# Kernel optimization log

Measured on AMD Instinct MI355X. Metric: run time of the kernel, lower is better.

## Reference

```python
import jax, jax.numpy as jnp
import numpy as np

EPS = 1e-13

def dct_basis(n):
    # Orthonormal DCT-II basis: C[k, i] = s_k * cos(pi*(2i+1)*k / (2n))
    k = np.arange(n)[:, None]
    i = np.arange(n)[None, :]
    C = np.cos(np.pi * (2 * i + 1) * k / (2 * n))
    scale = np.full((n, 1), np.sqrt(2.0 / n))
    scale[0, 0] = np.sqrt(1.0 / n)
    return jnp.asarray(C * scale, dtype=jnp.float32)


def setup_inputs() -> dict:
    key = jax.random.key(0)
    B, C, H, W = 128, 3, 256, 256
    inputs = jax.random.normal(key, (B, C, H, W), dtype=jnp.float32)
    mean = jnp.asarray(-8.0, dtype=jnp.float32)
    std = jnp.asarray(6.0, dtype=jnp.float32)
    return {"inputs": inputs, "mean": mean, "std": std}


def reference(inputs, mean, std):
    H, W = inputs.shape[-2], inputs.shape[-1]
    CH = dct_basis(H)  # [H, H]
    CW = dct_basis(W)  # [W, W]
    # 2D DCT-II (ortho): out[..., k1, k2] = sum_ij CH[k1,i] * x[..., i, j] * CW[k2,j]
    x = jnp.einsum('hi,bcij,wj->bchw', CH, inputs, CW)
    x = jnp.log(jnp.abs(x) + EPS)
    return (x - mean) / std
```

## Files before the change

### kernel.cpp

```cpp
#include <hip/hip_runtime.h>
#include <cmath>


#define HN    256
#define NIMG  384

__global__ void basis_init(float* __restrict__ Tdf) {
    int idx = blockIdx.x * 256 + threadIdx.x;
    int i = idx >> 8, k = idx & 255;
    double c = cos(M_PI * (2.0 * i + 1.0) * (double)k / 512.0);
    double s = (k == 0) ? sqrt(1.0 / 256.0) : sqrt(2.0 / 256.0);
    Tdf[idx] = (float)(c * s);
}

__global__ __launch_bounds__(256, 4) void t1_kernel(
    const float* __restrict__ X, const float* __restrict__ Tdf,
    float* __restrict__ T1)
{
    __shared__ float Xs[8][64];
    __shared__ float CHs[8][HN];

    const int t   = threadIdx.x;
    const int img = blockIdx.x >> 2;
    const int js  = (blockIdx.x & 3) * 64;
    const float* __restrict__ Xi = X + (size_t)img * (HN * HN);

    const int ci = t & 15;
    const int ib = t >> 4;

    float acc[4][4][4];
    #pragma unroll
    for (int s = 0; s < 4; ++s)
        #pragma unroll
        for (int r = 0; r < 4; ++r)
            #pragma unroll
            for (int jr = 0; jr < 4; ++jr) acc[s][r][jr] = 0.0f;

    for (int i0 = 0; i0 < HN; i0 += 8) {
        {
            int rr = t >> 5, cc = (t & 31) * 2;
            float2 v = *(const float2*)(Xi + (i0 + rr) * HN + js + cc);
            Xs[rr][cc] = v.x; Xs[rr][cc + 1] = v.y;
            #pragma unroll
            for (int rep = 0; rep < 2; ++rep) {
                int idx = rep * 1024 + t * 4;
                int row = idx >> 8, col = idx & 255;
                *(float4*)&CHs[row][col] =
                    *(const float4*)(Tdf + (i0 + row) * HN + col);
            }
        }
        __syncthreads();
        #pragma unroll
        for (int ii = 0; ii < 8; ++ii) {
            float xv[4];
            *(float4*)xv = *(const float4*)&Xs[ii][4 * ci];
            float ch[4][4];
            #pragma unroll
            for (int s = 0; s < 4; ++s)
                *(float4*)ch[s] = *(const float4*)&CHs[ii][64 * s + 4 * ib];
            #pragma unroll
            for (int s = 0; s < 4; ++s)
                #pragma unroll
                for (int r = 0; r < 4; ++r)
                    #pragma unroll
                    for (int jr = 0; jr < 4; ++jr)
                        acc[s][r][jr] = fmaf(ch[s][r], xv[jr], acc[s][r][jr]);
        }
        __syncthreads();
    }

    float* __restrict__ T1i = T1 + (size_t)img * (HN * HN);
    #pragma unroll
    for (int s = 0; s < 4; ++s)
        #pragma unroll
        for (int r = 0; r < 4; ++r)
            *(float4*)(T1i + (64 * s + 4 * ib + r) * HN + js + 4 * ci) =
                *(const float4*)acc[s][r];
}

__global__ __launch_bounds__(256, 4) void y_kernel(
    const float* __restrict__ T1, const float* __restrict__ Tdf,
    const float* __restrict__ meanp, const float* __restrict__ stdp,
    float* __restrict__ out)
{
    __shared__ float T1c[64][9];
    __shared__ float Bc[8][HN];

    const int t   = threadIdx.x;
    const int img = blockIdx.x >> 2;
    const int ks  = (blockIdx.x & 3) * 64;
    const float* __restrict__ T1i = T1 + (size_t)img * (HN * HN);

    const int ci = t & 15;
    const int ib = t >> 4;

    float acc[4][4][4];
    #pragma unroll
    for (int s = 0; s < 4; ++s)
        #pragma unroll
        for (int r = 0; r < 4; ++r)
            #pragma unroll
            for (int c = 0; c < 4; ++c) acc[s][r][c] = 0.0f;

    for (int j0 = 0; j0 < HN; j0 += 8) {
        {
            int rr = t >> 2, cc = (t & 3) * 2;
            float2 v = *(const float2*)(T1i + (ks + rr) * HN + j0 + cc);
            T1c[rr][cc] = v.x; T1c[rr][cc + 1] = v.y;
            #pragma unroll
            for (int rep = 0; rep < 2; ++rep) {
                int idx = rep * 1024 + t * 4;
                int row = idx >> 8, col = idx & 255;
                *(float4*)&Bc[row][col] =
                    *(const float4*)(Tdf + (j0 + row) * HN + col);
            }
        }
        __syncthreads();
        #pragma unroll
        for (int p = 0; p < 8; ++p) {
            float a[4];
            #pragma unroll
            for (int r = 0; r < 4; ++r) a[r] = T1c[4 * ib + r][p];
            float b[4][4];
            #pragma unroll
            for (int s = 0; s < 4; ++s)
                *(float4*)b[s] = *(const float4*)&Bc[p][64 * s + 4 * ci];
            #pragma unroll
            for (int s = 0; s < 4; ++s)
                #pragma unroll
                for (int r = 0; r < 4; ++r)
                    #pragma unroll
                    for (int c = 0; c < 4; ++c)
                        acc[s][r][c] = fmaf(a[r], b[s][c], acc[s][r][c]);
        }
        __syncthreads();
    }

    const float mean = meanp[0];
    const float stdv = stdp[0];
    float* __restrict__ O = out + (size_t)img * (HN * HN);
    #pragma unroll
    for (int s = 0; s < 4; ++s)
        #pragma unroll
        for (int r = 0; r < 4; ++r) {
            float4 v;
            v.x = (logf(fabsf(acc[s][r][0]) + 1e-13f) - mean) / stdv;
            v.y = (logf(fabsf(acc[s][r][1]) + 1e-13f) - mean) / stdv;
            v.z = (logf(fabsf(acc[s][r][2]) + 1e-13f) - mean) / stdv;
            v.w = (logf(fabsf(acc[s][r][3]) + 1e-13f) - mean) / stdv;
            *(float4*)(O + (ks + 4 * ib + r) * HN + 64 * s + 4 * ci) = v;
        }
}

#define SLAB 32
__global__ __launch_bounds__(256, 3) void dct2_f32(
    const float* __restrict__ X, const float* __restrict__ Tdf,
    const float* __restrict__ meanp, const float* __restrict__ stdp,
    float* __restrict__ out)
{
    __shared__ union SU {
        struct { float Xs[8][HN]; float CHc[8][SLAB]; } p1;
        float Bc[16][HN];
    } u;
    __shared__ float T1s[SLAB][HN + 1];

    const int t   = threadIdx.x;
    const int img = blockIdx.x >> 3;
    const int k0  = (blockIdx.x & 7) * SLAB;
    const float* __restrict__ Xi = X + (size_t)img * (HN * HN);
    const int ci = t & 7;
    const int ib = t >> 3;

    float acc[8][4];
    #pragma unroll
    for (int q = 0; q < 8; ++q)
        #pragma unroll
        for (int r = 0; r < 4; ++r) acc[q][r] = 0.0f;

    for (int i0 = 0; i0 < HN; i0 += 8) {
        {
            int rr = t >> 5, cc = (t & 31) * 4;
            float4 a = *(const float4*)(Xi + (i0 + rr) * HN + cc);
            float4 b = *(const float4*)(Xi + (i0 + rr) * HN + cc + 128);
            *(float4*)&u.p1.Xs[rr][cc]       = a;
            *(float4*)&u.p1.Xs[rr][cc + 128] = b;
            u.p1.CHc[rr][t & 31] = Tdf[(i0 + rr) * HN + k0 + (t & 31)];
        }
        __syncthreads();
        #pragma unroll
        for (int ii = 0; ii < 8; ++ii) {
            float xr[8];
            *(float4*)&xr[0] = *(const float4*)&u.p1.Xs[ii][8 * ib];
            *(float4*)&xr[4] = *(const float4*)&u.p1.Xs[ii][8 * ib + 4];
            float ch[4];
            *(float4*)&ch[0] = *(const float4*)&u.p1.CHc[ii][4 * ci];
            #pragma unroll
            for (int q = 0; q < 8; ++q)
                #pragma unroll
                for (int r = 0; r < 4; ++r)
                    acc[q][r] = fmaf(ch[r], xr[q], acc[q][r]);
        }
        __syncthreads();
    }
    #pragma unroll
    for (int q = 0; q < 8; ++q)
        #pragma unroll
        for (int r = 0; r < 4; ++r)
            T1s[4 * ci + r][8 * ib + q] = acc[q][r];
    __syncthreads();

    float acc2[8][4];
    #pragma unroll
    for (int q = 0; q < 8; ++q)
        #pragma unroll
        for (int r = 0; r < 4; ++r) acc2[q][r] = 0.0f;

    for (int j0 = 0; j0 < HN; j0 += 16) {
        #pragma unroll
        for (int rep = 0; rep < 4; ++rep) {
            int idx = rep * 1024 + t * 4;
            int p = idx >> 8, c = idx & 255;
            *(float4*)&u.Bc[p][c] = *(const float4*)(Tdf + (j0 + p) * HN + c);
        }
        __syncthreads();
        #pragma unroll
        for (int p = 0; p < 16; ++p) {
            float a[4];
            #pragma unroll
            for (int r = 0; r < 4; ++r) a[r] = T1s[4 * ci + r][j0 + p];
            float b[8];
            *(float4*)&b[0] = *(const float4*)&u.Bc[p][8 * ib];
            *(float4*)&b[4] = *(const float4*)&u.Bc[p][8 * ib + 4];
            #pragma unroll
            for (int q = 0; q < 8; ++q)
                #pragma unroll
                for (int r = 0; r < 4; ++r)
                    acc2[q][r] = fmaf(a[r], b[q], acc2[q][r]);
        }
        __syncthreads();
    }

    const float mean = meanp[0];
    const float stdv = stdp[0];
    #pragma unroll
    for (int q = 0; q < 8; ++q)
        #pragma unroll
        for (int r = 0; r < 4; ++r) {
            float v = (logf(fabsf(acc2[q][r]) + 1e-13f) - mean) / stdv;
            T1s[4 * ci + r][8 * ib + q] = v;
        }
    __syncthreads();

    float* __restrict__ O = out + (size_t)img * (HN * HN) + (size_t)k0 * HN;
    #pragma unroll
    for (int rep = 0; rep < 8; ++rep) {
        int idx = rep * 1024 + t * 4;
        int row = idx >> 8, col = idx & 255;
        float4 v = make_float4(T1s[row][col], T1s[row][col + 1],
                               T1s[row][col + 2], T1s[row][col + 3]);
        *(float4*)(O + row * HN + col) = v;
    }
}

extern "C" void kernel_launch(void* const* d_in, const int* in_sizes, int n_in,
                              void* d_out, int out_size, void* d_ws, size_t ws_size,
                              hipStream_t stream) {
    const float* X     = (const float*)d_in[0];
    const float* meanp = (const float*)d_in[1];
    const float* stdp  = (const float*)d_in[2];

    float* Tdf = (float*)d_ws;
    const size_t T1_OFF    = 256 * 1024;
    const size_t T1_BYTES  = (size_t)NIMG * HN * HN * sizeof(float);

    basis_init<<<256, 256, 0, stream>>>(Tdf);

    if (ws_size >= T1_OFF + T1_BYTES) {
        float* T1 = (float*)((char*)d_ws + T1_OFF);
        t1_kernel<<<NIMG * 4, 256, 0, stream>>>(X, Tdf, T1);
        y_kernel <<<NIMG * 4, 256, 0, stream>>>(T1, Tdf, meanp, stdp,
                                                (float*)d_out);
    } else {
        dct2_f32<<<NIMG * 8, 256, 0, stream>>>(X, Tdf, meanp, stdp,
                                               (float*)d_out);
    }
}
```

Measured before the change: 448.9 us.

## Register-prefetch next K-tile, double K-step to 16, transpose T1 tile in LDS

Both GEMM kernels now load the next K-slab from global memory into registers while the current slab in shared memory is being computed, with wider float4 global loads. The K step per iteration goes from 8 to 16, halving the number of barrier pairs. In y_kernel the T1 tile is stored transposed with padding so each thread reads its four A values with a single float4 LDS load. The cost is more registers for the prefetch buffers and a larger shared-memory footprint, which may reduce occupancy under the launch bounds of 4 blocks.

```diff
diff --git a/kernel.cpp b/kernel.cpp
--- a/kernel.cpp
+++ b/kernel.cpp
@@ -17,8 +17,8 @@
     const float* __restrict__ X, const float* __restrict__ Tdf,
     float* __restrict__ T1)
 {
-    __shared__ float Xs[8][64];
-    __shared__ float CHs[8][HN];
+    __shared__ float Xs[16][64];
+    __shared__ float CHs[16][HN];
 
     const int t   = threadIdx.x;
     const int img = blockIdx.x >> 2;
@@ -36,22 +36,33 @@
             #pragma unroll
             for (int jr = 0; jr < 4; ++jr) acc[s][r][jr] = 0.0f;
 
-    for (int i0 = 0; i0 < HN; i0 += 8) {
-        {
-            int rr = t >> 5, cc = (t & 31) * 2;
-            float2 v = *(const float2*)(Xi + (i0 + rr) * HN + js + cc);
-            Xs[rr][cc] = v.x; Xs[rr][cc + 1] = v.y;
-            #pragma unroll
-            for (int rep = 0; rep < 2; ++rep) {
-                int idx = rep * 1024 + t * 4;
-                int row = idx >> 8, col = idx & 255;
-                *(float4*)&CHs[row][col] =
-                    *(const float4*)(Tdf + (i0 + row) * HN + col);
-            }
-        }
-        __syncthreads();
-        #pragma unroll
-        for (int ii = 0; ii < 8; ++ii) {
+    float4 pX, pC[4];
+    const int xr_row = t >> 4, xr_col = (t & 15) * 4;
+    #define T1_PREFETCH(i0)                                                  \
+        do {                                                                 \
+            pX = *(const float4*)(Xi + ((i0) + xr_row) * HN + js + xr_col);  \
+            _Pragma("unroll")                                                \
+            for (int rep = 0; rep < 4; ++rep) {                              \
+                int idx = rep * 1024 + t * 4;                                \
+                pC[rep] = *(const float4*)(Tdf + ((i0) + (idx >> 8)) * HN    \
+                                           + (idx & 255));                   \
+            }                                                                \
+        } while (0)
+
+    T1_PREFETCH(0);
+    for (int i0 = 0; i0 < HN; i0 += 16) {
+        __syncthreads();
+        *(float4*)&Xs[xr_row][xr_col] = pX;
+        #pragma unroll
+        for (int rep = 0; rep < 4; ++rep) {
+            int idx = rep * 1024 + t * 4;
+            *(float4*)&CHs[idx >> 8][idx & 255] = pC[rep];
+        }
+        __syncthreads();
+        if (i0 + 16 < HN) T1_PREFETCH(i0 + 16);
+
+        #pragma unroll
+        for (int ii = 0; ii < 16; ++ii) {
             float xv[4];
             *(float4*)xv = *(const float4*)&Xs[ii][4 * ci];
             float ch[4][4];
@@ -66,8 +77,8 @@
                     for (int jr = 0; jr < 4; ++jr)
                         acc[s][r][jr] = fmaf(ch[s][r], xv[jr], acc[s][r][jr]);
         }
-        __syncthreads();
-    }
+    }
+    #undef T1_PREFETCH
 
     float* __restrict__ T1i = T1 + (size_t)img * (HN * HN);
     #pragma unroll
@@ -83,8 +94,8 @@
     const float* __restrict__ meanp, const float* __restrict__ stdp,
     float* __restrict__ out)
 {
-    __shared__ float T1c[64][9];
-    __shared__ float Bc[8][HN];
+    __shared__ float Ts[16][68];
+    __shared__ float Bc[16][HN];
 
     const int t   = threadIdx.x;
     const int img = blockIdx.x >> 2;
@@ -102,25 +113,38 @@
             #pragma unroll
             for (int c = 0; c < 4; ++c) acc[s][r][c] = 0.0f;
 
-    for (int j0 = 0; j0 < HN; j0 += 8) {
-        {
-            int rr = t >> 2, cc = (t & 3) * 2;
-            float2 v = *(const float2*)(T1i + (ks + rr) * HN + j0 + cc);
-            T1c[rr][cc] = v.x; T1c[rr][cc + 1] = v.y;
-            #pragma unroll
-            for (int rep = 0; rep < 2; ++rep) {
-                int idx = rep * 1024 + t * 4;
-                int row = idx >> 8, col = idx & 255;
-                *(float4*)&Bc[row][col] =
-                    *(const float4*)(Tdf + (j0 + row) * HN + col);
-            }
-        }
-        __syncthreads();
-        #pragma unroll
-        for (int p = 0; p < 8; ++p) {
+    float4 pT, pB[4];
+    const int tr_row = t >> 2, tr_col = (t & 3) * 4;
+    #define Y_PREFETCH(j0)                                                   \
+        do {                                                                 \
+            pT = *(const float4*)(T1i + (ks + tr_row) * HN + (j0) + tr_col); \
+            _Pragma("unroll")                                                \
+            for (int rep = 0; rep < 4; ++rep) {                              \
+                int idx = rep * 1024 + t * 4;                                \
+                pB[rep] = *(const float4*)(Tdf + ((j0) + (idx >> 8)) * HN    \
+                                           + (idx & 255));                   \
+            }                                                                \
+        } while (0)
+
+    Y_PREFETCH(0);
+    for (int j0 = 0; j0 < HN; j0 += 16) {
+        __syncthreads();
+        Ts[tr_col + 0][tr_row] = pT.x;
+        Ts[tr_col + 1][tr_row] = pT.y;
+        Ts[tr_col + 2][tr_row] = pT.z;
+        Ts[tr_col + 3][tr_row] = pT.w;
+        #pragma unroll
+        for (int rep = 0; rep < 4; ++rep) {
+            int idx = rep * 1024 + t * 4;
+            *(float4*)&Bc[idx >> 8][idx & 255] = pB[rep];
+        }
+        __syncthreads();
+        if (j0 + 16 < HN) Y_PREFETCH(j0 + 16);
+
+        #pragma unroll
+        for (int p = 0; p < 16; ++p) {
             float a[4];
-            #pragma unroll
-            for (int r = 0; r < 4; ++r) a[r] = T1c[4 * ib + r][p];
+            *(float4*)a = *(const float4*)&Ts[p][4 * ib];
             float b[4][4];
             #pragma unroll
             for (int s = 0; s < 4; ++s)
@@ -133,8 +157,8 @@
                     for (int c = 0; c < 4; ++c)
                         acc[s][r][c] = fmaf(a[r], b[s][c], acc[s][r][c]);
         }
-        __syncthreads();
-    }
+    }
+    #undef Y_PREFETCH
 
     const float mean = meanp[0];
     const float stdv = stdp[0];
```

Result: slower. 762.3 us (+69.8%).
